# Kernel optimization log

Hardware: AMD Instinct MI355X
Metric: run time of the kernel (lower is better)

## Reference

```python
import jax, jax.numpy as jnp
import numpy as np

GROUPS = 8
EPS = 1e-5


def setup_inputs() -> dict:
    key = jax.random.key(0)
    k1, k2, k3 = jax.random.split(key, 3)
    B, C, H, W = 4, 256, 64, 64
    x = jax.random.normal(k1, (B, C, H, W), dtype=jnp.float32)
    gamma = jnp.ones((C,), dtype=jnp.float32)
    beta = jnp.zeros((C,), dtype=jnp.float32)
    # conv1x1 weights flattened to [out, in]
    w_qkv = jax.random.normal(k2, (3 * C, C), dtype=jnp.float32) * (C ** -0.5)
    w_proj = jax.random.normal(k3, (C, C), dtype=jnp.float32) * (C ** -0.5)
    b_proj = jnp.zeros((C,), dtype=jnp.float32)
    return {"x": x, "gamma": gamma, "beta": beta, "w_qkv": w_qkv,
            "w_proj": w_proj, "b_proj": b_proj}


def group_norm(x, gamma, beta):
    B, C, H, W = x.shape
    xr = x.reshape(B, GROUPS, C // GROUPS, H * W)
    mu = xr.mean(axis=(2, 3), keepdims=True)
    var = xr.var(axis=(2, 3), keepdims=True)
    xn = (xr - mu) * jax.lax.rsqrt(var + EPS)
    xn = xn.reshape(B, C, H * W)
    return xn * gamma[None, :, None] + beta[None, :, None]


def reference(x, gamma, beta, w_qkv, w_proj, b_proj):
    B, C, H, W = x.shape
    N = H * W
    xn = group_norm(x, gamma, beta)               # [B, C, N]
    qkv = jnp.einsum('oc,bcn->bon', w_qkv, xn)    # [B, 3C, N]
    q, k, v = jnp.split(qkv, 3, axis=1)           # each [B, C, N]
    # attn[b, n, m] = sum_c q[b,c,n] * k[b,c,m] * C^-0.5
    scores = jnp.einsum('bcn,bcm->bnm', q, k) * (C ** -0.5)  # [B, N, N]
    attn = jax.nn.softmax(scores, axis=-1)
    # out = v @ attn^T  -> out[b,c,n] = sum_m v[b,c,m] * attn[b,n,m]
    out = jnp.einsum('bcm,bnm->bcn', v, attn)     # [B, C, N]
    y = jnp.einsum('oc,bcn->bon', w_proj, out) + b_proj[None, :, None]
    return x + y.reshape(B, C, H, W)
```

## Files before the change

### kernel.cpp

```cpp
#include <hip/hip_runtime.h>
#include <hip/hip_bf16.h>

#define BB 4
#define CC 256
#define NN 4096
#define GG 8
#define SPLITS 4
#define TKV 64
#define ITERS (NN / SPLITS / TKV)

typedef unsigned char u8;
typedef unsigned short u16;
typedef unsigned int u32;
typedef __bf16 b16x8 __attribute__((ext_vector_type(8)));
typedef float f32x4 __attribute__((ext_vector_type(4)));
typedef u32 u32x4 __attribute__((ext_vector_type(4)));
typedef u32 u32x2 __attribute__((ext_vector_type(2)));
typedef u16 u16x4 __attribute__((ext_vector_type(4)));

#define QS 0.09016844005556021f
#define FMAX 8.0f


__device__ __forceinline__ u16 f2bf(float f) {
    u32 u = __builtin_bit_cast(u32, f);
    u = (u + 0x7FFFu + ((u >> 16) & 1u)) >> 16;
    return (u16)u;
}

__device__ __forceinline__ float bf2f(u16 h) {
    return __builtin_bit_cast(float, (u32)h << 16);
}

__device__ __forceinline__ u32 pack_bf2(float a, float b) {
    float2 f; f.x = a; f.y = b;
    __hip_bfloat162 h = __float22bfloat162_rn(f);
    u32 r;
    __builtin_memcpy(&r, &h, 4);
    return r;
}

__device__ __forceinline__ float exp2_raw(float x) {
#if __has_builtin(__builtin_amdgcn_exp2f)
    return __builtin_amdgcn_exp2f(x);
#else
    float r;
    asm("v_exp_f32 %0, %1" : "=v"(r) : "v"(x));
    return r;
#endif
}

__device__ __forceinline__ b16x8 ldfrag(const u16* p) {
    u32x4 v = *reinterpret_cast<const u32x4*>(p);
    return __builtin_bit_cast(b16x8, v);
}

__device__ __forceinline__ int pk_fp8x4(float a, float b, float c, float d) {
    int r = __builtin_amdgcn_cvt_pk_fp8_f32(a, b, 0, false);
    r = __builtin_amdgcn_cvt_pk_fp8_f32(c, d, r, true);
    return r;
}

__device__ __forceinline__ long as_long(u32x2 v) { return __builtin_bit_cast(long, v); }

typedef __attribute__((address_space(1))) const unsigned int* gas_p;
typedef __attribute__((address_space(3))) unsigned int* las_p;

__device__ __forceinline__ void g2l(const u8* g, u8* l) {
    __builtin_amdgcn_global_load_lds((gas_p)g, (las_p)l, 16, 0, 0);
}

__device__ __forceinline__ void g2l16(const u16* g, u16* l) {
    __builtin_amdgcn_global_load_lds((gas_p)g, (las_p)l, 16, 0, 0);
}

__global__ void fold_w(const float* __restrict__ w_qkv, const float* __restrict__ w_proj,
                       const float* __restrict__ gamma, const float* __restrict__ beta,
                       const float* __restrict__ gsum,
                       u16* __restrict__ wqf, float* __restrict__ biasq,
                       u16* __restrict__ wpf) {
    int o = blockIdx.x;
    int b = blockIdx.y;
    int c = threadIdx.x;
    int g = c >> 5;
    const float inv = 1.f / ((CC / GG) * NN);
    float s  = gsum[(b * GG + g) * 2];
    float ss = gsum[(b * GG + g) * 2 + 1];
    float mu = s * inv;
    float rstd = rsqrtf(ss * inv - mu * mu + 1e-5f);
    float a  = gamma[c] * rstd;
    float bb = beta[c] - mu * a;
    float w = w_qkv[o * CC + c];
    size_t fe = ((size_t)((o >> 4) * 8 + (c >> 5)) * 64 + ((c & 31) >> 3) * 16 + (o & 15)) * 8 + (c & 7);
    wqf[(size_t)b * 768 * CC + fe] = f2bf(w * a);
    float part = w * bb;
    #pragma unroll
    for (int off = 32; off; off >>= 1) part += __shfl_down(part, off, 64);
    __shared__ float red[4];
    if ((threadIdx.x & 63) == 0) red[threadIdx.x >> 6] = part;
    __syncthreads();
    if (threadIdx.x == 0) biasq[b * 768 + o] = red[0] + red[1] + red[2] + red[3];
    if (b == 0 && o < CC) {
        float wp = w_proj[o * CC + c];
        wpf[fe] = f2bf(wp);
    }
}

__global__ void transpose_x(const float* __restrict__ x, u16* __restrict__ xtf,
                            float* __restrict__ gsum) {
    __shared__ float tile[64][65];
    __shared__ float red[4][4];
    int n0 = blockIdx.x * 64, c0 = blockIdx.y * 64, b = blockIdx.z;
    int t = threadIdx.x;
    int c4 = (t & 15) * 4;
    int r0 = t >> 4;
    const float* xp = x + (size_t)b * CC * NN;
    float s0 = 0.f, ss0 = 0.f, s1 = 0.f, ss1 = 0.f;
    #pragma unroll
    for (int i = 0; i < 4; ++i) {
        int row = i * 16 + r0;
        float4 v = *reinterpret_cast<const float4*>(&xp[(size_t)(c0 + row) * NN + n0 + c4]);
        tile[row][c4 + 0] = v.x; tile[row][c4 + 1] = v.y;
        tile[row][c4 + 2] = v.z; tile[row][c4 + 3] = v.w;
        float s = v.x + v.y + v.z + v.w;
        float q = v.x * v.x + v.y * v.y + v.z * v.z + v.w * v.w;
        if (i < 2) { s0 += s; ss0 += q; } else { s1 += s; ss1 += q; }
    }
    #pragma unroll
    for (int off = 32; off; off >>= 1) {
        s0 += __shfl_down(s0, off, 64); ss0 += __shfl_down(ss0, off, 64);
        s1 += __shfl_down(s1, off, 64); ss1 += __shfl_down(ss1, off, 64);
    }
    int wid = t >> 6;
    if ((t & 63) == 0) { red[wid][0] = s0; red[wid][1] = ss0; red[wid][2] = s1; red[wid][3] = ss1; }
    __syncthreads();
    if (t < 2) {
        float s  = red[0][t * 2] + red[1][t * 2] + red[2][t * 2] + red[3][t * 2];
        float ss = red[0][t * 2 + 1] + red[1][t * 2 + 1] + red[2][t * 2 + 1] + red[3][t * 2 + 1];
        int g = (c0 >> 5) + t;
        atomicAdd(&gsum[(b * GG + g) * 2], s);
        atomicAdd(&gsum[(b * GG + g) * 2 + 1], ss);
    }
    int nl = t >> 2;
    int cbq = t & 3;
    int l15 = nl & 15;
    int ntile = (n0 >> 4) + (nl >> 4);
    int kk = (c0 >> 5) + (cbq >> 1);
    u16* ob = xtf + (size_t)b * NN * CC;
    #pragma unroll
    for (int g = 0; g < 4; ++g) {
        int quad = (cbq & 1) * 2 + (g >> 1);
        int j0 = (g & 1) * 4;
        u16x4 v;
        v.x = f2bf(tile[cbq * 16 + g * 4 + 0][nl]);
        v.y = f2bf(tile[cbq * 16 + g * 4 + 1][nl]);
        v.z = f2bf(tile[cbq * 16 + g * 4 + 2][nl]);
        v.w = f2bf(tile[cbq * 16 + g * 4 + 3][nl]);
        *reinterpret_cast<u16x4*>(ob + ((size_t)(ntile * 8 + kk) * 64 + quad * 16 + l15) * 8 + j0) = v;
    }
}

__global__ void __launch_bounds__(256) qkv_gemm(const u16* __restrict__ wqf,
                                                const float* __restrict__ biasq,
                                                const u16* __restrict__ xtf,
                                                u8* __restrict__ qtf, u8* __restrict__ ktf,
                                                u8* __restrict__ vvf) {
    __shared__ u16 bx[16384];
    int b = blockIdx.z;
    int o0 = blockIdx.y * 128;
    int n0 = blockIdx.x * 64;
    int lane = threadIdx.x & 63, w = threadIdx.x >> 6;
    int l15 = lane & 15, quad = lane >> 4;
    const u16* Bg = xtf + (size_t)b * NN * CC + (size_t)n0 * 256;
    #pragma unroll
    for (int j = 0; j < 8; ++j) {
        int c = w * 8 + j;
        g2l16(Bg + (size_t)c * 512 + lane * 8, bx + (size_t)c * 512 + lane * 8);
    }
    __syncthreads();

    const u16* A = wqf + (size_t)b * 768 * CC;
    f32x4 acc[2][4] = {};
    #pragma unroll
    for (int kk = 0; kk < 8; ++kk) {
        b16x8 af[2];
        #pragma unroll
        for (int t = 0; t < 2; ++t) {
            int otile = (o0 >> 4) + w * 2 + t;
            af[t] = ldfrag(A + (size_t)(otile * 8 + kk) * 512 + lane * 8);
        }
        #pragma unroll
        for (int nt = 0; nt < 4; ++nt) {
            b16x8 bf = ldfrag(bx + (size_t)(nt * 8 + kk) * 512 + lane * 8);
            acc[0][nt] = __builtin_amdgcn_mfma_f32_16x16x32_bf16(af[0], bf, acc[0][nt], 0, 0, 0);
            acc[1][nt] = __builtin_amdgcn_mfma_f32_16x16x32_bf16(af[1], bf, acc[1][nt], 0, 0, 0);
        }
    }
    #pragma unroll
    for (int t = 0; t < 2; ++t) {
        int o_base = o0 + (w * 2 + t) * 16 + quad * 4;
        float bias[4];
        #pragma unroll
        for (int r = 0; r < 4; ++r) bias[r] = biasq[b * 768 + o_base + r];
        if (o0 < 512) {
            int oloc = (o0 < 256) ? o_base : (o_base - 256);
            u8* dst = ((o0 < 256) ? qtf : ktf) + (size_t)b * NN * CC;
            #pragma unroll
            for (int nt = 0; nt < 4; ++nt) {
                int n = n0 + nt * 16 + l15;
                int pk = pk_fp8x4(acc[t][nt][0] + bias[0], acc[t][nt][1] + bias[1],
                                  acc[t][nt][2] + bias[2], acc[t][nt][3] + bias[3]);
                size_t addr = (size_t)((n >> 4) * 4 + (oloc >> 6)) * 1024
                            + ((oloc & 31) >> 3) * 256 + (n & 15) * 16
                            + ((oloc >> 5) & 1) * 8 + (oloc & 7);
                *reinterpret_cast<u32*>(dst + addr) = (u32)pk;
            }
        } else {
            int cb = o_base - 512;
            u8* dst = vvf + (size_t)b * NN * CC;
            #pragma unroll
            for (int nt = 0; nt < 4; ++nt) {
                int kv = n0 + nt * 16 + l15;
                int pk = pk_fp8x4(acc[t][nt][0] + bias[0], acc[t][nt][1] + bias[1],
                                  acc[t][nt][2] + bias[2], acc[t][nt][3] + bias[3]);
                size_t base = (size_t)((kv >> 5) * 8 + (cb >> 5)) * 1024
                            + ((kv & 31) >> 3) * 256 + ((cb >> 4) & 1) * 8 + (kv & 7);
                #pragma unroll
                for (int r = 0; r < 4; ++r)
                    dst[base + ((cb & 15) + r) * 16] = (u8)(pk >> (r * 8));
            }
        }
    }
}

__global__ void __launch_bounds__(512, 4) flash(const u8* __restrict__ qtf,
                                                const u8* __restrict__ ktf,
                                                const u8* __restrict__ vvf,
                                                u16* __restrict__ po,
                                                float* __restrict__ lp) {
    __shared__ u8 kbuf[2][16384];
    __shared__ u8 vbuf[2][16384];
    __shared__ u8 pbuf[8][16 * 72];
    int lin = blockIdx.x;
    int chunk = lin & 15;
    int nblk = lin >> 4;
    int b = chunk >> 2, sp = chunk & 3;
    int lane = threadIdx.x & 63, w = threadIdx.x >> 6;
    int l15 = lane & 15, quad = lane >> 4;
    int ntile = nblk * 8 + w;
    const u8* kb8 = ktf + (size_t)b * NN * CC;
    const u8* vb8 = vvf + (size_t)b * NN * CC;
    u8* pw = &pbuf[w][0];

    const u32x2 ones2 = {0x38383838u, 0x38383838u};
    const long ones8 = as_long(ones2);

    u32x4 aq[4];
    const u8* qb = qtf + (size_t)b * NN * CC + (size_t)ntile * 4096;
    #pragma unroll
    for (int s = 0; s < 4; ++s)
        aq[s] = *reinterpret_cast<const u32x4*>(qb + s * 1024 + lane * 16);

    f32x4 acco[16] = {};
    f32x4 acco_l = {};

    const int m_beg = sp * (NN / SPLITS);

    auto stage = [&](int buf, int m0) {
        const u8* ks = kb8 + ((size_t)m0 << 8);
        const u8* vs = vb8 + ((size_t)m0 << 8);
        #pragma unroll
        for (int j = 0; j < 4; ++j) {
            int idx = w * 4 + j;
            if (idx < 16) g2l(ks + idx * 1024 + lane * 16, &kbuf[buf][idx * 1024]);
            else          g2l(vs + (idx - 16) * 1024 + lane * 16, &vbuf[buf][(idx - 16) * 1024]);
        }
    };

    stage(0, m_beg);
    __syncthreads();
    for (int it = 0; it < ITERS; ++it) {
        int cur = it & 1;
        if (it + 1 < ITERS) stage(cur ^ 1, m_beg + (it + 1) * TKV);
        const u8* kc = &kbuf[cur][0];
        const u8* vc = &vbuf[cur][0];
        f32x4 accs[4] = {};
        #pragma unroll
        for (int s = 0; s < 4; ++s) {
            long alo = as_long(u32x2{aq[s].x, aq[s].y});
            long ahi = as_long(u32x2{aq[s].z, aq[s].w});
            #pragma unroll
            for (int m = 0; m < 4; ++m) {
                u32x4 kf = *reinterpret_cast<const u32x4*>(kc + (size_t)(m * 4 + s) * 1024 + lane * 16);
                accs[m] = __builtin_amdgcn_mfma_f32_16x16x32_fp8_fp8(
                    alo, as_long(u32x2{kf.x, kf.y}), accs[m], 0, 0, 0);
                accs[m] = __builtin_amdgcn_mfma_f32_16x16x32_fp8_fp8(
                    ahi, as_long(u32x2{kf.z, kf.w}), accs[m], 0, 0, 0);
            }
        }
        #pragma unroll
        for (int m = 0; m < 4; ++m) {
            float e0 = exp2_raw(fmaf(accs[m][0], QS, -FMAX));
            float e1 = exp2_raw(fmaf(accs[m][1], QS, -FMAX));
            float e2 = exp2_raw(fmaf(accs[m][2], QS, -FMAX));
            float e3 = exp2_raw(fmaf(accs[m][3], QS, -FMAX));
            int p01 = __builtin_amdgcn_cvt_pk_fp8_f32(e0, e1, 0, false);
            int p23 = __builtin_amdgcn_cvt_pk_fp8_f32(e2, e3, 0, false);
            u8* pr = pw + m * 16 + l15;
            pr[(quad * 4 + 0) * 72] = (u8)p01;
            pr[(quad * 4 + 1) * 72] = (u8)(p01 >> 8);
            pr[(quad * 4 + 2) * 72] = (u8)p23;
            pr[(quad * 4 + 3) * 72] = (u8)(p23 >> 8);
        }
        asm volatile("s_waitcnt lgkmcnt(0)" ::: "memory");
        long ap0 = as_long(*reinterpret_cast<const u32x2*>(pw + l15 * 72 + quad * 8));
        long ap1 = as_long(*reinterpret_cast<const u32x2*>(pw + l15 * 72 + 32 + quad * 8));
        acco_l = __builtin_amdgcn_mfma_f32_16x16x32_fp8_fp8(ap0, ones8, acco_l, 0, 0, 0);
        acco_l = __builtin_amdgcn_mfma_f32_16x16x32_fp8_fp8(ap1, ones8, acco_l, 0, 0, 0);
        #pragma unroll
        for (int c2 = 0; c2 < 8; ++c2) {
            u32x4 vf0 = *reinterpret_cast<const u32x4*>(vc + (size_t)c2 * 1024 + lane * 16);
            u32x4 vf1 = *reinterpret_cast<const u32x4*>(vc + (size_t)(8 + c2) * 1024 + lane * 16);
            acco[c2 * 2]     = __builtin_amdgcn_mfma_f32_16x16x32_fp8_fp8(
                ap0, as_long(u32x2{vf0.x, vf0.y}), acco[c2 * 2], 0, 0, 0);
            acco[c2 * 2 + 1] = __builtin_amdgcn_mfma_f32_16x16x32_fp8_fp8(
                ap0, as_long(u32x2{vf0.z, vf0.w}), acco[c2 * 2 + 1], 0, 0, 0);
            acco[c2 * 2]     = __builtin_amdgcn_mfma_f32_16x16x32_fp8_fp8(
                ap1, as_long(u32x2{vf1.x, vf1.y}), acco[c2 * 2], 0, 0, 0);
            acco[c2 * 2 + 1] = __builtin_amdgcn_mfma_f32_16x16x32_fp8_fp8(
                ap1, as_long(u32x2{vf1.z, vf1.w}), acco[c2 * 2 + 1], 0, 0, 0);
        }
        __syncthreads();
    }
    u16* pochunk = po + ((size_t)(sp * BB + b) * 256 + ntile) * 4096;
    #pragma unroll
    for (int ct = 0; ct < 16; ++ct) {
        u32x2 st;
        st.x = pack_bf2(acco[ct][0], acco[ct][1]);
        st.y = pack_bf2(acco[ct][2], acco[ct][3]);
        *reinterpret_cast<u32x2*>(pochunk + (size_t)(ct * 64 + quad * 16 + l15) * 4) = st;
    }
    if (l15 == 0) {
        size_t lbase = (size_t)(sp * BB + b) * NN + ntile * 16;
        #pragma unroll
        for (int r = 0; r < 4; ++r) lp[lbase + quad * 4 + r] = acco_l[r];
    }
}

__global__ void __launch_bounds__(512) proj(const u16* __restrict__ wpf,
                                            const float* __restrict__ b_proj,
                                            const u16* __restrict__ po,
                                            const float* __restrict__ lp,
                                            const float* __restrict__ x,
                                            float* __restrict__ out) {
    __shared__ u16 bO[16384];
    int b = blockIdx.y, n0 = blockIdx.x * 64;
    int t = threadIdx.x;
    {
        int cg = t & 31, quad = (t >> 5) & 3, ntl = t >> 7;
        int nb = (n0 >> 4) + ntl;
        float acc[4][8] = {};
        float lsum[4] = {};
        #pragma unroll
        for (int s = 0; s < SPLITS; ++s) {
            const u16* src = po + (((size_t)(s * BB + b) * 256 + nb) * 4096)
                           + ((cg >> 1) * 256 + quad * 64 + (cg & 1) * 32);
            u16 s16[32];
            #pragma unroll
            for (int q = 0; q < 4; ++q)
                *reinterpret_cast<u32x4*>(&s16[q * 8]) = *reinterpret_cast<const u32x4*>(src + q * 8);
            #pragma unroll
            for (int r = 0; r < 4; ++r)
                #pragma unroll
                for (int j = 0; j < 8; ++j)
                    acc[r][j] += bf2f(s16[j * 4 + r]);
            #pragma unroll
            for (int r = 0; r < 4; ++r)
                lsum[r] += lp[(size_t)(s * BB + b) * NN + nb * 16 + quad * 4 + r];
        }
        #pragma unroll
        for (int r = 0; r < 4; ++r) {
            float inv = 1.f / lsum[r];
            u16 outv[8];
            #pragma unroll
            for (int j = 0; j < 8; ++j) outv[j] = f2bf(acc[r][j] * inv);
            size_t off = ((size_t)(ntl * 8 + (cg >> 2)) * 64 + (cg & 3) * 16 + quad * 4 + r) * 8;
            *reinterpret_cast<u32x4*>(bO + off) = *reinterpret_cast<const u32x4*>(outv);
        }
    }
    __syncthreads();
    int lane = t & 63, w = t >> 6;
    int l15 = lane & 15, quad = lane >> 4;
    f32x4 acc2[2][4] = {};
    #pragma unroll
    for (int kk = 0; kk < 8; ++kk) {
        b16x8 af[2];
        #pragma unroll
        for (int tt = 0; tt < 2; ++tt) {
            int otile = w * 2 + tt;
            af[tt] = ldfrag(wpf + (size_t)(otile * 8 + kk) * 512 + lane * 8);
        }
        #pragma unroll
        for (int nt = 0; nt < 4; ++nt) {
            b16x8 bf = ldfrag(bO + (size_t)(nt * 8 + kk) * 512 + lane * 8);
            acc2[0][nt] = __builtin_amdgcn_mfma_f32_16x16x32_bf16(af[0], bf, acc2[0][nt], 0, 0, 0);
            acc2[1][nt] = __builtin_amdgcn_mfma_f32_16x16x32_bf16(af[1], bf, acc2[1][nt], 0, 0, 0);
        }
    }
    #pragma unroll
    for (int tt = 0; tt < 2; ++tt) {
        int o_base = (w * 2 + tt) * 16 + quad * 4;
        #pragma unroll
        for (int nt = 0; nt < 4; ++nt) {
            int n = n0 + nt * 16 + l15;
            #pragma unroll
            for (int r = 0; r < 4; ++r) {
                int o = o_base + r;
                size_t idx = ((size_t)(b * CC + o)) * NN + n;
                out[idx] = acc2[tt][nt][r] + b_proj[o] + x[idx];
            }
        }
    }
}

extern "C" void kernel_launch(void* const* d_in, const int* in_sizes, int n_in,
                              void* d_out, int out_size, void* d_ws, size_t ws_size,
                              hipStream_t stream) {
    const float* x      = (const float*)d_in[0];
    const float* gamma  = (const float*)d_in[1];
    const float* beta   = (const float*)d_in[2];
    const float* w_qkv  = (const float*)d_in[3];
    const float* w_proj = (const float*)d_in[4];
    const float* b_proj = (const float*)d_in[5];
    float* out = (float*)d_out;

    char* p = (char*)d_ws;
    float* gsum  = (float*)p; p += 256;
    float* biasq = (float*)p; p += (size_t)BB * 768 * sizeof(float);
    u16* wqf = (u16*)p; p += (size_t)BB * 768 * CC * 2;
    u16* wpf = (u16*)p; p += (size_t)CC * CC * 2;
    u16* xtf = (u16*)p; p += (size_t)BB * NN * CC * 2;
    u8* qtf8 = (u8*)p; p += (size_t)BB * NN * CC;
    u8* ktf8 = (u8*)p; p += (size_t)BB * NN * CC;
    u8* vvf8 = (u8*)p; p += (size_t)BB * NN * CC;
    u16* po = (u16*)p; p += (size_t)SPLITS * BB * NN * CC * 2;
    float* lp = (float*)p; p += (size_t)SPLITS * BB * NN * sizeof(float);
    (void)ws_size; (void)in_sizes; (void)n_in; (void)out_size;

    (void)hipMemsetAsync(gsum, 0, BB * GG * 2 * sizeof(float), stream);
    transpose_x<<<dim3(NN / 64, CC / 64, BB), 256, 0, stream>>>(x, xtf, gsum);
    fold_w<<<dim3(768, BB), 256, 0, stream>>>(w_qkv, w_proj, gamma, beta, gsum, wqf, biasq, wpf);
    qkv_gemm<<<dim3(NN / 64, 6, BB), 256, 0, stream>>>(wqf, biasq, xtf, qtf8, ktf8, vvf8);
    flash<<<(NN / 128) * SPLITS * BB, 512, 0, stream>>>(qtf8, ktf8, vvf8, po, lp);
    proj<<<dim3(NN / 64, BB), 512, 0, stream>>>(wpf, b_proj, po, lp, x, out);
}
```

Before: 174.1 us.

## Transpose flash MFMA operands to pass P via bpermute instead of LDS

The QK^T and PV MFMAs swap operand order so the score tile lands in a layout where probabilities can be moved between lanes with ds_bpermute, without a per-wave LDS round trip and waitcnt. Row sums are accumulated in scalar floats from the unquantized exponentials and reduced with shuffles, replacing the ones-matrix MFMA. The proj kernel's partial-output reduction is reworked to match the new transposed po layout. Row sums now come from fp32 values rather than fp8-rounded ones, which slightly changes numerics relative to the numerator.

After: 179.6 us. 3.1% more time.

```diff
diff --git a/kernel.cpp b/kernel.cpp
--- a/kernel.cpp
+++ b/kernel.cpp
@@ -240,7 +240,6 @@
                                                 float* __restrict__ lp) {
     __shared__ u8 kbuf[2][16384];
     __shared__ u8 vbuf[2][16384];
-    __shared__ u8 pbuf[8][16 * 72];
     int lin = blockIdx.x;
     int chunk = lin & 15;
     int nblk = lin >> 4;
@@ -250,10 +249,10 @@
     int ntile = nblk * 8 + w;
     const u8* kb8 = ktf + (size_t)b * NN * CC;
     const u8* vb8 = vvf + (size_t)b * NN * CC;
-    u8* pw = &pbuf[w][0];
-
-    const u32x2 ones2 = {0x38383838u, 0x38383838u};
-    const long ones8 = as_long(ones2);
+
+    const int idx_lo = (l15 + ((lane & 16) << 1)) << 2;
+    const int idx_hi = idx_lo + 64;
+    const bool qlt2 = quad < 2;
 
     u32x4 aq[4];
     const u8* qb = qtf + (size_t)b * NN * CC + (size_t)ntile * 4096;
@@ -262,7 +261,7 @@
         aq[s] = *reinterpret_cast<const u32x4*>(qb + s * 1024 + lane * 16);
 
     f32x4 acco[16] = {};
-    f32x4 acco_l = {};
+    float lsum = 0.f;
 
     const int m_beg = sp * (NN / SPLITS);
 
@@ -287,48 +286,45 @@
         f32x4 accs[4] = {};
         #pragma unroll
         for (int s = 0; s < 4; ++s) {
-            long alo = as_long(u32x2{aq[s].x, aq[s].y});
-            long ahi = as_long(u32x2{aq[s].z, aq[s].w});
+            long qlo = as_long(u32x2{aq[s].x, aq[s].y});
+            long qhi = as_long(u32x2{aq[s].z, aq[s].w});
             #pragma unroll
             for (int m = 0; m < 4; ++m) {
                 u32x4 kf = *reinterpret_cast<const u32x4*>(kc + (size_t)(m * 4 + s) * 1024 + lane * 16);
                 accs[m] = __builtin_amdgcn_mfma_f32_16x16x32_fp8_fp8(
-                    alo, as_long(u32x2{kf.x, kf.y}), accs[m], 0, 0, 0);
+                    as_long(u32x2{kf.x, kf.y}), qlo, accs[m], 0, 0, 0);
                 accs[m] = __builtin_amdgcn_mfma_f32_16x16x32_fp8_fp8(
-                    ahi, as_long(u32x2{kf.z, kf.w}), accs[m], 0, 0, 0);
-            }
-        }
+                    as_long(u32x2{kf.z, kf.w}), qhi, accs[m], 0, 0, 0);
+            }
+        }
+        int pk[4];
         #pragma unroll
         for (int m = 0; m < 4; ++m) {
             float e0 = exp2_raw(fmaf(accs[m][0], QS, -FMAX));
             float e1 = exp2_raw(fmaf(accs[m][1], QS, -FMAX));
             float e2 = exp2_raw(fmaf(accs[m][2], QS, -FMAX));
             float e3 = exp2_raw(fmaf(accs[m][3], QS, -FMAX));
-            int p01 = __builtin_amdgcn_cvt_pk_fp8_f32(e0, e1, 0, false);
-            int p23 = __builtin_amdgcn_cvt_pk_fp8_f32(e2, e3, 0, false);
-            u8* pr = pw + m * 16 + l15;
-            pr[(quad * 4 + 0) * 72] = (u8)p01;
-            pr[(quad * 4 + 1) * 72] = (u8)(p01 >> 8);
-            pr[(quad * 4 + 2) * 72] = (u8)p23;
-            pr[(quad * 4 + 3) * 72] = (u8)(p23 >> 8);
-        }
-        asm volatile("s_waitcnt lgkmcnt(0)" ::: "memory");
-        long ap0 = as_long(*reinterpret_cast<const u32x2*>(pw + l15 * 72 + quad * 8));
-        long ap1 = as_long(*reinterpret_cast<const u32x2*>(pw + l15 * 72 + 32 + quad * 8));
-        acco_l = __builtin_amdgcn_mfma_f32_16x16x32_fp8_fp8(ap0, ones8, acco_l, 0, 0, 0);
-        acco_l = __builtin_amdgcn_mfma_f32_16x16x32_fp8_fp8(ap1, ones8, acco_l, 0, 0, 0);
-        #pragma unroll
-        for (int c2 = 0; c2 < 8; ++c2) {
-            u32x4 vf0 = *reinterpret_cast<const u32x4*>(vc + (size_t)c2 * 1024 + lane * 16);
-            u32x4 vf1 = *reinterpret_cast<const u32x4*>(vc + (size_t)(8 + c2) * 1024 + lane * 16);
-            acco[c2 * 2]     = __builtin_amdgcn_mfma_f32_16x16x32_fp8_fp8(
-                ap0, as_long(u32x2{vf0.x, vf0.y}), acco[c2 * 2], 0, 0, 0);
-            acco[c2 * 2 + 1] = __builtin_amdgcn_mfma_f32_16x16x32_fp8_fp8(
-                ap0, as_long(u32x2{vf0.z, vf0.w}), acco[c2 * 2 + 1], 0, 0, 0);
-            acco[c2 * 2]     = __builtin_amdgcn_mfma_f32_16x16x32_fp8_fp8(
-                ap1, as_long(u32x2{vf1.x, vf1.y}), acco[c2 * 2], 0, 0, 0);
-            acco[c2 * 2 + 1] = __builtin_amdgcn_mfma_f32_16x16x32_fp8_fp8(
-                ap1, as_long(u32x2{vf1.z, vf1.w}), acco[c2 * 2 + 1], 0, 0, 0);
+            lsum += (e0 + e1) + (e2 + e3);
+            pk[m] = pk_fp8x4(e0, e1, e2, e3);
+        }
+        #pragma unroll
+        for (int h = 0; h < 2; ++h) {
+            int pe = pk[2 * h], pd = pk[2 * h + 1];
+            int lo_e = __builtin_amdgcn_ds_bpermute(idx_lo, pe);
+            int lo_d = __builtin_amdgcn_ds_bpermute(idx_lo, pd);
+            int hi_e = __builtin_amdgcn_ds_bpermute(idx_hi, pe);
+            int hi_d = __builtin_amdgcn_ds_bpermute(idx_hi, pd);
+            u32 blo = qlt2 ? (u32)lo_e : (u32)lo_d;
+            u32 bhi = qlt2 ? (u32)hi_e : (u32)hi_d;
+            long bop = as_long(u32x2{blo, bhi});
+            #pragma unroll
+            for (int c2 = 0; c2 < 8; ++c2) {
+                u32x4 vf = *reinterpret_cast<const u32x4*>(vc + (size_t)(h * 8 + c2) * 1024 + lane * 16);
+                acco[c2 * 2]     = __builtin_amdgcn_mfma_f32_16x16x32_fp8_fp8(
+                    as_long(u32x2{vf.x, vf.y}), bop, acco[c2 * 2], 0, 0, 0);
+                acco[c2 * 2 + 1] = __builtin_amdgcn_mfma_f32_16x16x32_fp8_fp8(
+                    as_long(u32x2{vf.z, vf.w}), bop, acco[c2 * 2 + 1], 0, 0, 0);
+            }
         }
         __syncthreads();
     }
@@ -340,11 +336,10 @@
         st.y = pack_bf2(acco[ct][2], acco[ct][3]);
         *reinterpret_cast<u32x2*>(pochunk + (size_t)(ct * 64 + quad * 16 + l15) * 4) = st;
     }
-    if (l15 == 0) {
-        size_t lbase = (size_t)(sp * BB + b) * NN + ntile * 16;
-        #pragma unroll
-        for (int r = 0; r < 4; ++r) lp[lbase + quad * 4 + r] = acco_l[r];
-    }
+    lsum += __shfl_xor(lsum, 16, 64);
+    lsum += __shfl_xor(lsum, 32, 64);
+    if (lane < 16)
+        lp[(size_t)(sp * BB + b) * NN + ntile * 16 + l15] = lsum;
 }
 
 __global__ void __launch_bounds__(512) proj(const u16* __restrict__ wpf,
@@ -357,35 +352,40 @@
     int b = blockIdx.y, n0 = blockIdx.x * 64;
     int t = threadIdx.x;
     {
-        int cg = t & 31, quad = (t >> 5) & 3, ntl = t >> 7;
+        int u = t & 127, ntl = t >> 7;
         int nb = (n0 >> 4) + ntl;
-        float acc[4][8] = {};
-        float lsum[4] = {};
+        int a = u & 7;
+        int cblk = u >> 3;
+        float accn[2][16] = {};
+        float lsum2[2] = {};
         #pragma unroll
         for (int s = 0; s < SPLITS; ++s) {
             const u16* src = po + (((size_t)(s * BB + b) * 256 + nb) * 4096)
-                           + ((cg >> 1) * 256 + quad * 64 + (cg & 1) * 32);
-            u16 s16[32];
-            #pragma unroll
-            for (int q = 0; q < 4; ++q)
-                *reinterpret_cast<u32x4*>(&s16[q * 8]) = *reinterpret_cast<const u32x4*>(src + q * 8);
-            #pragma unroll
-            for (int r = 0; r < 4; ++r)
+                           + cblk * 256 + a * 8;
+            #pragma unroll
+            for (int q4 = 0; q4 < 4; ++q4) {
+                u16 s16[8];
+                *reinterpret_cast<u32x4*>(s16) = *reinterpret_cast<const u32x4*>(src + q4 * 64);
                 #pragma unroll
-                for (int j = 0; j < 8; ++j)
-                    acc[r][j] += bf2f(s16[j * 4 + r]);
-            #pragma unroll
-            for (int r = 0; r < 4; ++r)
-                lsum[r] += lp[(size_t)(s * BB + b) * NN + nb * 16 + quad * 4 + r];
-        }
-        #pragma unroll
-        for (int r = 0; r < 4; ++r) {
-            float inv = 1.f / lsum[r];
-            u16 outv[8];
-            #pragma unroll
-            for (int j = 0; j < 8; ++j) outv[j] = f2bf(acc[r][j] * inv);
-            size_t off = ((size_t)(ntl * 8 + (cg >> 2)) * 64 + (cg & 3) * 16 + quad * 4 + r) * 8;
-            *reinterpret_cast<u32x4*>(bO + off) = *reinterpret_cast<const u32x4*>(outv);
+                for (int k = 0; k < 8; ++k)
+                    accn[k >> 2][q4 * 4 + (k & 3)] += bf2f(s16[k]);
+            }
+            lsum2[0] += lp[(size_t)(s * BB + b) * NN + nb * 16 + a * 2];
+            lsum2[1] += lp[(size_t)(s * BB + b) * NN + nb * 16 + a * 2 + 1];
+        }
+        #pragma unroll
+        for (int nsel = 0; nsel < 2; ++nsel) {
+            float inv = 1.f / lsum2[nsel];
+            int row = a * 2 + nsel;
+            #pragma unroll
+            for (int h = 0; h < 2; ++h) {
+                u16 outv[8];
+                #pragma unroll
+                for (int j = 0; j < 8; ++j) outv[j] = f2bf(accn[nsel][h * 8 + j] * inv);
+                int kk = cblk >> 1, quad_f = (cblk & 1) * 2 + h;
+                size_t off = ((size_t)(ntl * 8 + kk) * 64 + quad_f * 16 + row) * 8;
+                *reinterpret_cast<u32x4*>(bO + off) = *reinterpret_cast<const u32x4*>(outv);
+            }
         }
     }
     __syncthreads();
```
